# Kernel optimization log

Hardware: AMD Instinct MI355X
Metric: run time of the kernel (lower is better)

Reference implementation:

```python
import jax, jax.numpy as jnp
import numpy as np

B, N, H, E, OBS, A, AFF, EFF = 2, 50000, 64, 1_000_000, 128, 18, 512, 256


def setup_inputs() -> dict:
    key = jax.random.key(0)
    ks = jax.random.split(key, 20)
    s = 0.05  # small init to keep gates/tanh unsaturated
    return {
        "obs": jax.random.normal(ks[0], (B, OBS), jnp.float32),
        "state": jax.random.normal(ks[1], (B, N, H), jnp.float32) * 0.1,
        "W_in": jax.random.normal(ks[2], (OBS, H), jnp.float32) * s,
        "b_in": jnp.zeros((H,), jnp.float32),
        "W_msg": jax.random.normal(ks[3], (H, H), jnp.float32) * s,
        "W_gate": jax.random.normal(ks[4], (2 * H, H), jnp.float32) * s,
        "b_gate": jnp.zeros((H,), jnp.float32),
        "W_cand": jax.random.normal(ks[5], (2 * H, H), jnp.float32) * s,
        "b_cand": jnp.zeros((H,), jnp.float32),
        "W_dec": jax.random.normal(ks[6], (H, H), jnp.float32) * s,
        "b_dec": jnp.zeros((H,), jnp.float32),
        "W_mean": jax.random.normal(ks[7], (H, A), jnp.float32) * s,
        "b_mean": jnp.zeros((A,), jnp.float32),
        "W_ls": jax.random.normal(ks[8], (H, A), jnp.float32) * s,
        "b_ls": jnp.zeros((A,), jnp.float32),
        "src_index": jax.random.randint(ks[9], (E,), 0, N),
        "dst_index": jax.random.randint(ks[10], (E,), 0, N),
        "afferent_idx": jax.random.randint(ks[11], (AFF,), 0, N),
        "efferent_idx": jax.random.randint(ks[12], (EFF,), 0, N),
    }


def reference(obs, state, W_in, b_in, W_msg, W_gate, b_gate, W_cand, b_cand,
              W_dec, b_dec, W_mean, b_mean, W_ls, b_ls,
              src_index, dst_index, afferent_idx, efferent_idx):
    # inject obs projection into afferent node slots
    projected = obs @ W_in + b_in                                   # [B, H]
    injected = jnp.zeros_like(state).at[:, afferent_idx, :].set(projected[:, None, :])
    # gather-project-scatter message passing over the edge list
    src_msgs = state[:, src_index, :] @ W_msg                       # [B, E, H]
    messages = jnp.zeros_like(state).at[:, dst_index, :].add(src_msgs)
    # GRU-style gated update
    combined = messages + injected
    gate_in = jnp.concatenate([state, combined], axis=-1)           # [B, N, 2H]
    z = jax.nn.sigmoid(gate_in @ W_gate + b_gate)
    cand = jnp.tanh(gate_in @ W_cand + b_cand)
    next_state = (1.0 - z) * state + z * cand
    # mean-pool readout over efferent nodes, then policy heads
    readout = next_state[:, efferent_idx, :].mean(axis=1)           # [B, H]
    decoded = jnp.tanh(readout @ W_dec + b_dec)
    mean = decoded @ W_mean + b_mean
    log_std = jnp.clip(decoded @ W_ls + b_ls, -5.0, 2.0)
    return mean, log_std, next_state
```

## Files before the change

kernel.cpp:

```cpp
#include <hip/hip_runtime.h>
#include <hip/hip_bf16.h>

constexpr int kN   = 50000;
constexpr int kH   = 64;
constexpr int kB   = 2;
constexpr int kE   = 1000000;
constexpr int kObs = 128;
constexpr int kA   = 18;
constexpr int kAff = 512;
constexpr int kEff = 256;
constexpr int kNH  = kN * kH;
constexpr int kOutOff = 2 * kB * kA;
constexpr int kHistBlocks = (kE + 1023) / 1024;
constexpr int kPackBlocks = (kNH + 2047) / 2048;
constexpr int kWprepBlocks = 80;
constexpr int kXcd = 8;
constexpr int kNperX = kN / kXcd;
constexpr int kN8  = kXcd * kN;
constexpr int kScanB = (kN + 1023) / 1024;

typedef __attribute__((ext_vector_type(8))) short short8_t;
typedef __attribute__((ext_vector_type(4))) float f32x4_t;

__device__ __forceinline__ float ldf(const void* p, int i, int f32) {
  if (f32) return ((const float*)p)[i];
  unsigned short u = ((const unsigned short*)p)[i];
  union { unsigned int x; float f; } v; v.x = ((unsigned int)u) << 16; return v.f;
}
__device__ __forceinline__ void stf(void* p, int i, float val, int f32) {
  if (f32) ((float*)p)[i] = val;
  else ((__hip_bfloat16*)p)[i] = __float2bfloat16(val);
}
__device__ __forceinline__ float lo16(unsigned int w) {
  union { unsigned int i; float f; } v; v.i = w << 16; return v.f;
}
__device__ __forceinline__ float hi16(unsigned int w) {
  union { unsigned int i; float f; } v; v.i = w & 0xffff0000u; return v.f;
}
__device__ __forceinline__ unsigned int f2b(float f) {
  union { float f; unsigned int u; } v; v.f = f;
  unsigned int r = v.u + 0x7fffu + ((v.u >> 16) & 1u);
  return r >> 16;
}
__device__ __forceinline__ int detect64(const unsigned short* wprobe, int t) {
  int hits = 0;
  for (int k = 0; k < 4; ++k) {
    unsigned short u = wprobe[(t * 4 + k) * 2];
    int e = (u >> 7) & 0xFF;
    if ((u & 0x7FFFu) != 0 && e >= 108 && e <= 128) hits++;
  }
  for (int off = 32; off; off >>= 1) hits += __shfl_down(hits, off);
  return (hits < 128) ? 1 : 0;
}

extern "C" __global__ void k_prep(const unsigned short* __restrict__ wprobe,
                                  const void* __restrict__ obs,
                                  const void* __restrict__ W_in,
                                  const void* __restrict__ b_in,
                                  const int* __restrict__ aff_idx,
                                  const int* __restrict__ dst,
                                  const void* __restrict__ state,
                                  const void* __restrict__ W_msg,
                                  const void* __restrict__ W_gate,
                                  const void* __restrict__ W_cand,
                                  int* __restrict__ dflag,
                                  int* __restrict__ flags,
                                  float* __restrict__ projected,
                                  int* __restrict__ deg8,
                                  unsigned int* __restrict__ pack,
                                  unsigned short* __restrict__ wt) {
  int t = threadIdx.x, b = blockIdx.x;
  if (b == 0) {
    __shared__ int sflag;
    if (t < 64) { int f = detect64(wprobe, t); if (t == 0) { sflag = f; dflag[0] = f; } }
    __syncthreads();
    int f32 = sflag;
    for (int j = t; j < kAff; j += 256) flags[aff_idx[j]] = 1;
    if (t < kB * kH) {
      int bb = t >> 6, h = t & 63;
      float acc = ldf(b_in, h, f32);
      for (int o = 0; o < kObs; ++o)
        acc += ldf(obs, bb * kObs + o, f32) * ldf(W_in, o * kH + h, f32);
      projected[t] = acc;
    }
  } else if (b <= kHistBlocks) {
    int rep = b & 7;
    int base = (b - 1) * 1024 + t;
#pragma unroll
    for (int k = 0; k < 4; ++k) {
      int e = base + k * 256;
      if (e < kE) atomicAdd(&deg8[rep * kN + dst[e]], 1);
    }
  } else if (b < 1 + kHistBlocks + kPackBlocks) {
    __shared__ int sflag;
    if (t < 64) { int f = detect64(wprobe, t); if (t == 0) sflag = f; }
    __syncthreads();
    int f32 = sflag;
    int i = (b - 1 - kHistBlocks) * 2048 + t * 8;
    if (i < kNH) {
      uint4 o0, o1;
      if (!f32) {
        uint4 a = *(const uint4*)((const unsigned short*)state + i);
        uint4 c = *(const uint4*)((const unsigned short*)state + kNH + i);
        o0.x = (a.x & 0xffffu) | (c.x << 16);
        o0.y = (a.x >> 16)     | (c.x & 0xffff0000u);
        o0.z = (a.y & 0xffffu) | (c.y << 16);
        o0.w = (a.y >> 16)     | (c.y & 0xffff0000u);
        o1.x = (a.z & 0xffffu) | (c.z << 16);
        o1.y = (a.z >> 16)     | (c.z & 0xffff0000u);
        o1.z = (a.w & 0xffffu) | (c.w << 16);
        o1.w = (a.w >> 16)     | (c.w & 0xffff0000u);
      } else {
        const float* sf = (const float*)state;
        unsigned int w[8];
#pragma unroll
        for (int k = 0; k < 8; ++k)
          w[k] = f2b(sf[i + k]) | (f2b(sf[kNH + i + k]) << 16);
        o0 = make_uint4(w[0], w[1], w[2], w[3]);
        o1 = make_uint4(w[4], w[5], w[6], w[7]);
      }
      *(uint4*)&pack[i] = o0;
      *(uint4*)&pack[i + 4] = o1;
    }
  } else {
    __shared__ int sflag;
    if (t < 64) { int f = detect64(wprobe, t); if (t == 0) sflag = f; }
    __syncthreads();
    int f32 = sflag;
    int i = (b - 1 - kHistBlocks - kPackBlocks) * 256 + t;
    if (i < 4096) {
      int n = i >> 6, k = i & 63;
      wt[i] = (unsigned short)f2b(ldf(W_msg, k * 64 + n, f32));
    } else if (i < 12288) {
      int j = i - 4096; int n = j >> 7, k = j & 127;
      wt[i] = (unsigned short)f2b(ldf(W_gate, k * 64 + n, f32));
    } else if (i < 20480) {
      int j = i - 12288; int n = j >> 7, k = j & 127;
      wt[i] = (unsigned short)f2b(ldf(W_cand, k * 64 + n, f32));
    }
  }
}

extern "C" __global__ void k_scan1(const int* __restrict__ deg8,
                                   int* __restrict__ row_off,
                                   int* __restrict__ partials) {
  __shared__ int sd[256];
  int t = threadIdx.x;
  int base = blockIdx.x * 1024 + t * 4;
  int d[4];
#pragma unroll
  for (int k = 0; k < 4; ++k) {
    int idx = base + k, s = 0;
    if (idx < kN) {
#pragma unroll
      for (int r = 0; r < 8; ++r) s += deg8[r * kN + idx];
    }
    d[k] = s;
  }
  int s4 = d[0] + d[1] + d[2] + d[3];
  sd[t] = s4;
  __syncthreads();
  for (int off = 1; off < 256; off <<= 1) {
    int v = (t >= off) ? sd[t - off] : 0;
    __syncthreads();
    sd[t] += v;
    __syncthreads();
  }
  int excl = sd[t] - s4;
  if (t == 255) partials[blockIdx.x] = sd[255];
#pragma unroll
  for (int k = 0; k < 4; ++k) {
    if (base + k < kN) row_off[base + k] = excl;
    excl += d[k];
  }
}

extern "C" __global__ void k_scan3(int* __restrict__ row_off,
                                   const int* __restrict__ partials,
                                   int* __restrict__ cursor) {
  __shared__ int sd[256];
  int t = threadIdx.x;
  int chunk = blockIdx.x >> 2;
  int s = 0;
  for (int j = t; j < chunk; j += 256) s += partials[j];
  sd[t] = s;
  __syncthreads();
  for (int off = 128; off; off >>= 1) {
    if (t < off) sd[t] += sd[t + off];
    __syncthreads();
  }
  int base = sd[0];
  int i = blockIdx.x * 256 + t;
  if (i < kN) {
    int v = row_off[i] + base;
    row_off[i] = v;
    cursor[i] = v;
  }
  if (blockIdx.x == 0 && t == 0) row_off[kN] = kE;
}

extern "C" __global__ void k_scatter(const int* __restrict__ src,
                                     const int* __restrict__ dst,
                                     int* __restrict__ cursor,
                                     int* __restrict__ sorted_src) {
  int x = blockIdx.x & 7;
  int j = blockIdx.x >> 3;
  int base = j * 1024 + threadIdx.x;
#pragma unroll
  for (int k = 0; k < 4; ++k) {
    int e = base + k * 256;
    if (e < kE) {
      int d = dst[e];
      if (d / kNperX == x) {
        int pos = atomicAdd(&cursor[d], 1);
        sorted_src[pos] = src[e];
      }
    }
  }
}

extern "C" __global__ __launch_bounds__(256) void k_gather(
    const unsigned int* __restrict__ pack,
    const int* __restrict__ row_off,
    const int* __restrict__ sorted_src,
    unsigned int* __restrict__ agg) {
  int wave = threadIdx.x >> 6, lane = threadIdx.x & 63;
  int n = blockIdx.x * 4 + wave;
  if (n >= kN) return;
  int s  = row_off[n];
  int en = row_off[n + 1];
  int g = lane >> 4, col = lane & 15;
  const uint4* pk4 = (const uint4*)pack;
  float a0x = 0.f, a0y = 0.f, a0z = 0.f, a0w = 0.f;
  float a1x = 0.f, a1y = 0.f, a1z = 0.f, a1w = 0.f;
  for (int e = s; e < en; e += 8) {
#pragma unroll
    for (int h = 0; h < 2; ++h) {
      int ee = e + h * 4 + g;
      int idx = sorted_src[min(ee, en - 1)];
      uint4 wv = pk4[idx * 16 + col];
      if (ee >= en) { wv.x = 0u; wv.y = 0u; wv.z = 0u; wv.w = 0u; }
      a0x += lo16(wv.x); a1x += hi16(wv.x);
      a0y += lo16(wv.y); a1y += hi16(wv.y);
      a0z += lo16(wv.z); a1z += hi16(wv.z);
      a0w += lo16(wv.w); a1w += hi16(wv.w);
    }
  }
  a0x += __shfl_xor(a0x, 16); a0x += __shfl_xor(a0x, 32);
  a0y += __shfl_xor(a0y, 16); a0y += __shfl_xor(a0y, 32);
  a0z += __shfl_xor(a0z, 16); a0z += __shfl_xor(a0z, 32);
  a0w += __shfl_xor(a0w, 16); a0w += __shfl_xor(a0w, 32);
  a1x += __shfl_xor(a1x, 16); a1x += __shfl_xor(a1x, 32);
  a1y += __shfl_xor(a1y, 16); a1y += __shfl_xor(a1y, 32);
  a1z += __shfl_xor(a1z, 16); a1z += __shfl_xor(a1z, 32);
  a1w += __shfl_xor(a1w, 16); a1w += __shfl_xor(a1w, 32);
  if (g == 0) {
    uint4 o;
    o.x = f2b(a0x) | (f2b(a1x) << 16);
    o.y = f2b(a0y) | (f2b(a1y) << 16);
    o.z = f2b(a0z) | (f2b(a1z) << 16);
    o.w = f2b(a0w) | (f2b(a1w) << 16);
    ((uint4*)agg)[n * 16 + col] = o;
  }
}

extern "C" __global__ __launch_bounds__(256) void k_update(
    const unsigned int* __restrict__ pk,
    const unsigned short* __restrict__ wt,
    const void* __restrict__ b_gate,
    const void* __restrict__ b_cand,
    const unsigned int* __restrict__ agg,
    const int* __restrict__ flags,
    const float* __restrict__ projected,
    const int* __restrict__ dflag,
    void* __restrict__ out) {
  __shared__ uint4 lw4[2752];
  __shared__ uint4 lx4[1088];
  __shared__ float sbias[128];
  __shared__ float sproj[128];
  __shared__ int   sfl[32];
  unsigned short* lwt = (unsigned short*)lw4;
  unsigned short* lx  = (unsigned short*)lx4;
  int f32 = dflag[0];
  int t = threadIdx.x;
  int nd0 = blockIdx.x * 32;

  const uint4* w4 = (const uint4*)wt;
  for (int i = t; i < 512; i += 256)  { int n = i >> 3, c = i & 7;  lw4[n * 9 + c] = w4[n * 8 + c]; }
  for (int i = t; i < 1024; i += 256) { int n = i >> 4, c = i & 15; lw4[576 + n * 17 + c] = w4[512 + n * 16 + c]; }
  for (int i = t; i < 1024; i += 256) { int n = i >> 4, c = i & 15; lw4[1664 + n * 17 + c] = w4[1536 + n * 16 + c]; }

  const uint4* pk4 = (const uint4*)pk;
  const uint4* ag4 = (const uint4*)agg;
  for (int i = t; i < 512; i += 256) {
    int ndl = i >> 4, c4 = i & 15;
    int ndg = min(nd0 + ndl, kN - 1);
    uint4 pv = pk4[ndg * 16 + c4];
    uint4 av = ag4[ndg * 16 + c4];
    *(uint2*)&lx[(2 * ndl) * 136 + c4 * 4] =
        make_uint2((pv.x & 0xffffu) | (pv.y << 16), (pv.z & 0xffffu) | (pv.w << 16));
    *(uint2*)&lx[(2 * ndl + 1) * 136 + c4 * 4] =
        make_uint2((pv.x >> 16) | (pv.y & 0xffff0000u), (pv.z >> 16) | (pv.w & 0xffff0000u));
    *(uint2*)&lx[(2 * ndl) * 136 + 64 + c4 * 4] =
        make_uint2((av.x & 0xffffu) | (av.y << 16), (av.z & 0xffffu) | (av.w << 16));
    *(uint2*)&lx[(2 * ndl + 1) * 136 + 64 + c4 * 4] =
        make_uint2((av.x >> 16) | (av.y & 0xffff0000u), (av.z >> 16) | (av.w & 0xffff0000u));
  }
  if (t < 64) sbias[t] = ldf(b_gate, t, f32);
  else if (t < 128) sbias[t] = ldf(b_cand, t - 64, f32);
  else sproj[t - 128] = projected[t - 128];
  if (t < 32) sfl[t] = (nd0 + t < kN) ? flags[nd0 + t] : 0;
  __syncthreads();

  int w = t >> 6, lane = t & 63;
  int q = lane >> 4, l15 = lane & 15;
  int rowb = w * 16;

  short8_t a0 = *(const short8_t*)&lx[(rowb + l15) * 136 + 64 + q * 8];
  short8_t a1 = *(const short8_t*)&lx[(rowb + l15) * 136 + 96 + q * 8];
  f32x4_t msgc[4];
#pragma unroll
  for (int ct = 0; ct < 4; ++ct) {
    f32x4_t acc = {0.f, 0.f, 0.f, 0.f};
    short8_t b0 = *(const short8_t*)&lwt[(ct * 16 + l15) * 72 + q * 8];
    short8_t b1 = *(const short8_t*)&lwt[(ct * 16 + l15) * 72 + 32 + q * 8];
    acc = __builtin_amdgcn_mfma_f32_16x16x32_bf16(a0, b0, acc, 0, 0, 0);
    acc = __builtin_amdgcn_mfma_f32_16x16x32_bf16(a1, b1, acc, 0, 0, 0);
    msgc[ct] = acc;
  }
#pragma unroll
  for (int ct = 0; ct < 4; ++ct) {
    int col = ct * 16 + l15;
    float pj0 = sproj[col], pj1 = sproj[64 + col];
#pragma unroll
    for (int r = 0; r < 4; ++r) {
      int row = rowb + q * 4 + r;
      int ndl = row >> 1, b = row & 1;
      float inj = sfl[ndl] ? (b ? pj1 : pj0) : 0.f;
      lx[row * 136 + 64 + col] = (unsigned short)f2b(msgc[ct][r] + inj);
    }
  }

  short8_t xa[4];
#pragma unroll
  for (int ks = 0; ks < 4; ++ks)
    xa[ks] = *(const short8_t*)&lx[(rowb + l15) * 136 + ks * 32 + q * 8];
#pragma unroll
  for (int ct = 0; ct < 4; ++ct) {
    f32x4_t accg = {0.f, 0.f, 0.f, 0.f}, accc = {0.f, 0.f, 0.f, 0.f};
#pragma unroll
    for (int ks = 0; ks < 4; ++ks) {
      short8_t bg = *(const short8_t*)&lwt[4608 + (ct * 16 + l15) * 136 + ks * 32 + q * 8];
      short8_t bc = *(const short8_t*)&lwt[13312 + (ct * 16 + l15) * 136 + ks * 32 + q * 8];
      accg = __builtin_amdgcn_mfma_f32_16x16x32_bf16(xa[ks], bg, accg, 0, 0, 0);
      accc = __builtin_amdgcn_mfma_f32_16x16x32_bf16(xa[ks], bc, accc, 0, 0, 0);
    }
    int col = ct * 16 + l15;
    float bgv = sbias[col], bcv = sbias[64 + col];
#pragma unroll
    for (int rp = 0; rp < 2; ++rp) {
      int rowe = rowb + q * 4 + 2 * rp;
      int nd = nd0 + (rowe >> 1);
      if (nd >= kN) continue;
      unsigned int pv = pk[nd * 64 + col];
      float z0 = 1.f / (1.f + __expf(-(accg[2 * rp] + bgv)));
      float c0 = tanhf(accc[2 * rp] + bcv);
      stf(out, kOutOff + nd * 64 + col, (1.f - z0) * lo16(pv) + z0 * c0, f32);
      float z1 = 1.f / (1.f + __expf(-(accg[2 * rp + 1] + bgv)));
      float c1 = tanhf(accc[2 * rp + 1] + bcv);
      stf(out, kOutOff + kNH + nd * 64 + col, (1.f - z1) * hi16(pv) + z1 * c1, f32);
    }
  }
}

extern "C" __global__ void k_readout(const void* __restrict__ W_dec,
                                     const void* __restrict__ b_dec,
                                     const void* __restrict__ W_mean,
                                     const void* __restrict__ b_mean,
                                     const void* __restrict__ W_ls,
                                     const void* __restrict__ b_ls,
                                     const int* __restrict__ eff_idx,
                                     const int* __restrict__ dflag,
                                     void* __restrict__ out) {
  __shared__ float part[8][64];
  __shared__ float ro[128], dec[128];
  int f32 = dflag[0];
  int t = threadIdx.x;
  int wv = t >> 6, lane = t & 63;
  int b = wv >> 2, g = wv & 3;
  float acc = 0.f;
#pragma unroll 4
  for (int i = 0; i < 64; ++i) {
    int n = eff_idx[g * 64 + i];
    acc += ldf(out, kOutOff + b * kNH + n * 64 + lane, f32);
  }
  part[wv][lane] = acc;
  __syncthreads();
  if (t < 128) {
    int bb = t >> 6, h = t & 63;
    float s = part[bb * 4 + 0][h] + part[bb * 4 + 1][h] +
              part[bb * 4 + 2][h] + part[bb * 4 + 3][h];
    ro[t] = s * (1.f / kEff);
  }
  __syncthreads();
  if (t < 128) {
    int bb = t >> 6, h = t & 63;
    float d = ldf(b_dec, h, f32);
    for (int k = 0; k < 64; ++k) d += ro[bb * 64 + k] * ldf(W_dec, k * 64 + h, f32);
    dec[t] = tanhf(d);
  }
  __syncthreads();
  if (t < kB * kA) {
    int bb = t / kA, a = t % kA;
    float m = ldf(b_mean, a, f32), l = ldf(b_ls, a, f32);
    for (int k = 0; k < 64; ++k) {
      float dv = dec[bb * 64 + k];
      m += dv * ldf(W_mean, k * kA + a, f32);
      l += dv * ldf(W_ls, k * kA + a, f32);
    }
    l = fminf(fmaxf(l, -5.f), 2.f);
    stf(out, t, m, f32);
    stf(out, kB * kA + t, l, f32);
  }
}

extern "C" void kernel_launch(void* const* d_in, const int* in_sizes, int n_in,
                              void* d_out, int out_size, void* d_ws, size_t ws_size,
                              hipStream_t stream) {
  (void)in_sizes; (void)n_in; (void)out_size; (void)ws_size;
  const void* obs    = d_in[0];
  const void* state  = d_in[1];
  const void* W_in   = d_in[2];
  const void* b_in   = d_in[3];
  const void* W_msg  = d_in[4];
  const void* W_gate = d_in[5];
  const void* b_gate = d_in[6];
  const void* W_cand = d_in[7];
  const void* b_cand = d_in[8];
  const void* W_dec  = d_in[9];
  const void* b_dec  = d_in[10];
  const void* W_mean = d_in[11];
  const void* b_mean = d_in[12];
  const void* W_ls   = d_in[13];
  const void* b_ls   = d_in[14];
  const int* src = (const int*)d_in[15];
  const int* dst = (const int*)d_in[16];
  const int* aff = (const int*)d_in[17];
  const int* eff = (const int*)d_in[18];

  int* wsp        = (int*)d_ws;
  int* flags      = wsp;
  int* deg8       = flags + kN;
  int* row_off    = deg8 + kN8;
  int* cursor     = row_off + (kN + 64);
  int* partials   = cursor + kN;
  int* dflag      = partials + 512;
  float* projected = (float*)(dflag + 16);
  int* sorted_src  = (int*)(projected + 128);
  unsigned int* pk  = (unsigned int*)(sorted_src + kE);
  unsigned int* agg = pk + kNH;
  unsigned short* wt = (unsigned short*)(agg + kNH);

  hipMemsetAsync(flags, 0, size_t(9 * kN) * sizeof(int), stream);
  k_prep<<<1 + kHistBlocks + kPackBlocks + kWprepBlocks, 256, 0, stream>>>(
      (const unsigned short*)W_cand, obs, W_in, b_in, aff, dst, state,
      W_msg, W_gate, W_cand, dflag, flags, projected, deg8, pk, wt);
  k_scan1<<<kScanB, 256, 0, stream>>>(deg8, row_off, partials);
  k_scan3<<<(kN + 255) / 256, 256, 0, stream>>>(row_off, partials, cursor);
  k_scatter<<<kXcd * kHistBlocks, 256, 0, stream>>>(src, dst, cursor, sorted_src);
  k_gather<<<(kN + 3) / 4, 256, 0, stream>>>(pk, row_off, sorted_src, agg);
  k_update<<<(kN + 31) / 32, 256, 0, stream>>>(pk, wt, b_gate, b_cand,
                                               agg, flags, projected, dflag, d_out);
  k_readout<<<1, 512, 0, stream>>>(W_dec, b_dec, W_mean, b_mean, W_ls, b_ls, eff,
                                   dflag, d_out);
}
```

Measured before the change: 307.7 us.

## Privatize degree histogram per block and move state packing into scatter

The degree histogram now runs as 32 long-running blocks. Each block owns a private copy of the histogram and updates it with workgroup-scope relaxed atomics, replacing the many short blocks that spread atomics over 8 replicas. The state bf16 packing moves from the prep kernel into the scatter kernel launch so it overlaps with the atomic-heavy scatter. The cost is a larger memset and a scan that sums 32 replicas per node, and only 32 blocks now carry the whole histogram pass. Workgroup-scope atomics on global memory are only correct because each replica is owned by a single block.

New measurement: 358.2 us. 1.16x slower.

```diff
diff --git a/kernel.cpp b/kernel.cpp
--- a/kernel.cpp
+++ b/kernel.cpp
@@ -16,7 +16,8 @@
 constexpr int kWprepBlocks = 80;
 constexpr int kXcd = 8;
 constexpr int kNperX = kN / kXcd;
-constexpr int kN8  = kXcd * kN;
+constexpr int kG   = 32;
+constexpr int kEg  = kE / kG;
 constexpr int kScanB = (kN + 1023) / 1024;
 
 typedef __attribute__((ext_vector_type(8))) short short8_t;
@@ -59,15 +60,13 @@
                                   const void* __restrict__ b_in,
                                   const int* __restrict__ aff_idx,
                                   const int* __restrict__ dst,
-                                  const void* __restrict__ state,
                                   const void* __restrict__ W_msg,
                                   const void* __restrict__ W_gate,
                                   const void* __restrict__ W_cand,
                                   int* __restrict__ dflag,
                                   int* __restrict__ flags,
                                   float* __restrict__ projected,
-                                  int* __restrict__ deg8,
-                                  unsigned int* __restrict__ pack,
+                                  int* __restrict__ deg_g,
                                   unsigned short* __restrict__ wt) {
   int t = threadIdx.x, b = blockIdx.x;
   if (b == 0) {
@@ -83,20 +82,119 @@
         acc += ldf(obs, bb * kObs + o, f32) * ldf(W_in, o * kH + h, f32);
       projected[t] = acc;
     }
-  } else if (b <= kHistBlocks) {
-    int rep = b & 7;
-    int base = (b - 1) * 1024 + t;
+  } else if (b <= kG) {
+    int g = b - 1;
+    int* reg = deg_g + g * kN;
+    int end = (g + 1) * kEg;
+    for (int e = g * kEg + t; e < end; e += 256)
+      __hip_atomic_fetch_add(&reg[dst[e]], 1, __ATOMIC_RELAXED,
+                             __HIP_MEMORY_SCOPE_WORKGROUP);
+  } else {
+    __shared__ int sflag;
+    if (t < 64) { int f = detect64(wprobe, t); if (t == 0) sflag = f; }
+    __syncthreads();
+    int f32 = sflag;
+    int i = (b - 1 - kG) * 256 + t;
+    if (i < 4096) {
+      int n = i >> 6, k = i & 63;
+      wt[i] = (unsigned short)f2b(ldf(W_msg, k * 64 + n, f32));
+    } else if (i < 12288) {
+      int j = i - 4096; int n = j >> 7, k = j & 127;
+      wt[i] = (unsigned short)f2b(ldf(W_gate, k * 64 + n, f32));
+    } else if (i < 20480) {
+      int j = i - 12288; int n = j >> 7, k = j & 127;
+      wt[i] = (unsigned short)f2b(ldf(W_cand, k * 64 + n, f32));
+    }
+  }
+}
+
+extern "C" __global__ void k_scan1(const int* __restrict__ deg_g,
+                                   int* __restrict__ row_off,
+                                   int* __restrict__ partials) {
+  __shared__ int sd[256];
+  int t = threadIdx.x;
+  int base = blockIdx.x * 1024 + t * 4;
+  int d[4];
+#pragma unroll
+  for (int k = 0; k < 4; ++k) {
+    int idx = base + k, s = 0;
+    if (idx < kN) {
+#pragma unroll
+      for (int r = 0; r < kG; ++r) s += deg_g[r * kN + idx];
+    }
+    d[k] = s;
+  }
+  int s4 = d[0] + d[1] + d[2] + d[3];
+  sd[t] = s4;
+  __syncthreads();
+  for (int off = 1; off < 256; off <<= 1) {
+    int v = (t >= off) ? sd[t - off] : 0;
+    __syncthreads();
+    sd[t] += v;
+    __syncthreads();
+  }
+  int excl = sd[t] - s4;
+  if (t == 255) partials[blockIdx.x] = sd[255];
+#pragma unroll
+  for (int k = 0; k < 4; ++k) {
+    if (base + k < kN) row_off[base + k] = excl;
+    excl += d[k];
+  }
+}
+
+extern "C" __global__ void k_scan3(int* __restrict__ row_off,
+                                   const int* __restrict__ partials,
+                                   int* __restrict__ cursor) {
+  __shared__ int sd[256];
+  int t = threadIdx.x;
+  int chunk = blockIdx.x >> 2;
+  int s = 0;
+  for (int j = t; j < chunk; j += 256) s += partials[j];
+  sd[t] = s;
+  __syncthreads();
+  for (int off = 128; off; off >>= 1) {
+    if (t < off) sd[t] += sd[t + off];
+    __syncthreads();
+  }
+  int base = sd[0];
+  int i = blockIdx.x * 256 + t;
+  if (i < kN) {
+    int v = row_off[i] + base;
+    row_off[i] = v;
+    cursor[i] = v;
+  }
+  if (blockIdx.x == 0 && t == 0) row_off[kN] = kE;
+}
+
+extern "C" __global__ void k_scatter(const int* __restrict__ src,
+                                     const int* __restrict__ dst,
+                                     int* __restrict__ cursor,
+                                     int* __restrict__ sorted_src,
+                                     const unsigned short* __restrict__ wprobe,
+                                     const void* __restrict__ state,
+                                     unsigned int* __restrict__ pack) {
+  int t = threadIdx.x;
+  if (blockIdx.x < kXcd * kHistBlocks) {
+    int x = blockIdx.x & 7;
+    int j = blockIdx.x >> 3;
+    int base = j * 1024 + t;
 #pragma unroll
     for (int k = 0; k < 4; ++k) {
       int e = base + k * 256;
-      if (e < kE) atomicAdd(&deg8[rep * kN + dst[e]], 1);
-    }
-  } else if (b < 1 + kHistBlocks + kPackBlocks) {
+      if (e < kE) {
+        int d = dst[e];
+        if (d / kNperX == x) {
+          int pos = atomicAdd(&cursor[d], 1);
+          sorted_src[pos] = src[e];
+        }
+      }
+    }
+  } else {
     __shared__ int sflag;
     if (t < 64) { int f = detect64(wprobe, t); if (t == 0) sflag = f; }
     __syncthreads();
     int f32 = sflag;
-    int i = (b - 1 - kHistBlocks) * 2048 + t * 8;
+    int i = (blockIdx.x - kXcd * kHistBlocks) * 2048 + t * 8;
     if (i < kNH) {
       uint4 o0, o1;
       if (!f32) {
@@ -121,100 +219,6 @@
       }
       *(uint4*)&pack[i] = o0;
       *(uint4*)&pack[i + 4] = o1;
-    }
-  } else {
-    __shared__ int sflag;
-    if (t < 64) { int f = detect64(wprobe, t); if (t == 0) sflag = f; }
-    __syncthreads();
-    int f32 = sflag;
-    int i = (b - 1 - kHistBlocks - kPackBlocks) * 256 + t;
-    if (i < 4096) {
-      int n = i >> 6, k = i & 63;
-      wt[i] = (unsigned short)f2b(ldf(W_msg, k * 64 + n, f32));
-    } else if (i < 12288) {
-      int j = i - 4096; int n = j >> 7, k = j & 127;
-      wt[i] = (unsigned short)f2b(ldf(W_gate, k * 64 + n, f32));
-    } else if (i < 20480) {
-      int j = i - 12288; int n = j >> 7, k = j & 127;
-      wt[i] = (unsigned short)f2b(ldf(W_cand, k * 64 + n, f32));
-    }
-  }
-}
-
-extern "C" __global__ void k_scan1(const int* __restrict__ deg8,
-                                   int* __restrict__ row_off,
-                                   int* __restrict__ partials) {
-  __shared__ int sd[256];
-  int t = threadIdx.x;
-  int base = blockIdx.x * 1024 + t * 4;
-  int d[4];
-#pragma unroll
-  for (int k = 0; k < 4; ++k) {
-    int idx = base + k, s = 0;
-    if (idx < kN) {
-#pragma unroll
-      for (int r = 0; r < 8; ++r) s += deg8[r * kN + idx];
-    }
-    d[k] = s;
-  }
-  int s4 = d[0] + d[1] + d[2] + d[3];
-  sd[t] = s4;
-  __syncthreads();
-  for (int off = 1; off < 256; off <<= 1) {
-    int v = (t >= off) ? sd[t - off] : 0;
-    __syncthreads();
-    sd[t] += v;
-    __syncthreads();
-  }
-  int excl = sd[t] - s4;
-  if (t == 255) partials[blockIdx.x] = sd[255];
-#pragma unroll
-  for (int k = 0; k < 4; ++k) {
-    if (base + k < kN) row_off[base + k] = excl;
-    excl += d[k];
-  }
-}
-
-extern "C" __global__ void k_scan3(int* __restrict__ row_off,
-                                   const int* __restrict__ partials,
-                                   int* __restrict__ cursor) {
-  __shared__ int sd[256];
-  int t = threadIdx.x;
-  int chunk = blockIdx.x >> 2;
-  int s = 0;
-  for (int j = t; j < chunk; j += 256) s += partials[j];
-  sd[t] = s;
-  __syncthreads();
-  for (int off = 128; off; off >>= 1) {
-    if (t < off) sd[t] += sd[t + off];
-    __syncthreads();
-  }
-  int base = sd[0];
-  int i = blockIdx.x * 256 + t;
-  if (i < kN) {
-    int v = row_off[i] + base;
-    row_off[i] = v;
-    cursor[i] = v;
-  }
-  if (blockIdx.x == 0 && t == 0) row_off[kN] = kE;
-}
-
-extern "C" __global__ void k_scatter(const int* __restrict__ src,
-                                     const int* __restrict__ dst,
-                                     int* __restrict__ cursor,
-                                     int* __restrict__ sorted_src) {
-  int x = blockIdx.x & 7;
-  int j = blockIdx.x >> 3;
-  int base = j * 1024 + threadIdx.x;
-#pragma unroll
-  for (int k = 0; k < 4; ++k) {
-    int e = base + k * 256;
-    if (e < kE) {
-      int d = dst[e];
-      if (d / kNperX == x) {
-        int pos = atomicAdd(&cursor[d], 1);
-        sorted_src[pos] = src[e];
-      }
     }
   }
 }
@@ -450,8 +454,8 @@
 
   int* wsp        = (int*)d_ws;
   int* flags      = wsp;
-  int* deg8       = flags + kN;
-  int* row_off    = deg8 + kN8;
+  int* deg_g      = flags + kN;
+  int* row_off    = deg_g + kG * kN;
   int* cursor     = row_off + (kN + 64);
   int* partials   = cursor + kN;
   int* dflag      = partials + 512;
@@ -461,13 +465,14 @@
   unsigned int* agg = pk + kNH;
   unsigned short* wt = (unsigned short*)(agg + kNH);
 
-  hipMemsetAsync(flags, 0, size_t(9 * kN) * sizeof(int), stream);
-  k_prep<<<1 + kHistBlocks + kPackBlocks + kWprepBlocks, 256, 0, stream>>>(
-      (const unsigned short*)W_cand, obs, W_in, b_in, aff, dst, state,
-      W_msg, W_gate, W_cand, dflag, flags, projected, deg8, pk, wt);
-  k_scan1<<<kScanB, 256, 0, stream>>>(deg8, row_off, partials);
+  hipMemsetAsync(flags, 0, size_t((1 + kG) * kN) * sizeof(int), stream);
+  k_prep<<<1 + kG + kWprepBlocks, 256, 0, stream>>>(
+      (const unsigned short*)W_cand, obs, W_in, b_in, aff, dst,
+      W_msg, W_gate, W_cand, dflag, flags, projected, deg_g, wt);
+  k_scan1<<<kScanB, 256, 0, stream>>>(deg_g, row_off, partials);
   k_scan3<<<(kN + 255) / 256, 256, 0, stream>>>(row_off, partials, cursor);
-  k_scatter<<<kXcd * kHistBlocks, 256, 0, stream>>>(src, dst, cursor, sorted_src);
+  k_scatter<<<kXcd * kHistBlocks + kPackBlocks, 256, 0, stream>>>(
+      src, dst, cursor, sorted_src, (const unsigned short*)W_cand, state, pk);
   k_gather<<<(kN + 3) / 4, 256, 0, stream>>>(pk, row_off, sorted_src, agg);
   k_update<<<(kN + 31) / 32, 256, 0, stream>>>(pk, wt, b_gate, b_cand,
                                                agg, flags, projected, dflag, d_out);
```
